# Optimization experiments

Hardware: AMD Instinct MI355X
Metric: run time of the kernel (lower is better)

Reference implementation:

```python
import jax, jax.numpy as jnp
import numpy as np

FACTOR = 2  # upsample factor per spatial dim


def setup_inputs() -> dict:
    key = jax.random.key(0)
    k1, k2, k3 = jax.random.split(key, 3)
    B, C_in, C_out, H, W_ = 8, 128, 128, 64, 64
    x = jax.random.normal(k1, (B, C_in, H, W_), dtype=jnp.float32)
    # conv3x3 params (OIHW), fan-in scaled init like torch Conv2d default scale
    fan_in = C_in * 3 * 3
    W = jax.random.normal(k2, (C_out, C_in, 3, 3), dtype=jnp.float32) / np.sqrt(fan_in)
    b = jax.random.normal(k3, (C_out,), dtype=jnp.float32) * 0.01
    return {"x": x, "W": W, "b": b}


def reference(x, W, b):
    h = jnp.repeat(jnp.repeat(x, FACTOR, axis=2), FACTOR, axis=3)  # [B,C,2H,2W]
    # conv3x3: stride 1, padding 1
    out = jax.lax.conv_general_dilated(
        h, W,
        window_strides=(1, 1),
        padding=((1, 1), (1, 1)),
        dimension_numbers=("NCHW", "OIHW", "NCHW"),
    )
    return out + b[None, :, None, None]
```

## Files before the change

kernel.cpp:

```cpp
#include <hip/hip_runtime.h>
#include <stdint.h>

typedef short bf16x8 __attribute__((ext_vector_type(8)));
typedef float f32x4 __attribute__((ext_vector_type(4)));
typedef float f32x16 __attribute__((ext_vector_type(16)));

#define NCI 128
#define NCO 128
#define HIN 64
#define NB  8

__device__ __forceinline__ unsigned short f32_to_bf16(float f) {
    union { float f; uint32_t u; } v; v.f = f;
    return (unsigned short)((v.u + 0x7FFFu + ((v.u >> 16) & 1u)) >> 16);
}

__device__ __forceinline__ void gl_lds16(const void* g, void* l) {
    __builtin_amdgcn_global_load_lds(
        (const __attribute__((address_space(1))) unsigned int*)g,
        (__attribute__((address_space(3))) unsigned int*)l, 16, 0, 0);
}

__device__ __forceinline__ float weff_sum(const float* wp, int py, int px, int ty, int tx) {
    float s = 0.f;
    #pragma unroll
    for (int ky = 0; ky < 3; ++ky) {
        bool iy = (py == 0) ? (ty == 0 ? (ky == 0) : (ky >= 1))
                            : (ty == 0 ? (ky <= 1) : (ky == 2));
        if (!iy) continue;
        #pragma unroll
        for (int kx = 0; kx < 3; ++kx) {
            bool ix = (px == 0) ? (tx == 0 ? (kx == 0) : (kx >= 1))
                                : (tx == 0 ? (kx <= 1) : (kx == 2));
            if (ix) s += wp[ky * 3 + kx];
        }
    }
    return s;
}

__global__ __launch_bounds__(256) void prep_kernel(
        const float* __restrict__ W, const float* __restrict__ x,
        unsigned short* __restrict__ Aw9, unsigned short* __restrict__ xq) {
    if (blockIdx.x < 1024) {
        int idx = blockIdx.x * 256 + threadIdx.x;
        int e   = idx & 7;
        int l   = (idx >> 3) & 63;
        int fm  = (idx >> 9) & 1;
        int s   = (idx >> 10) & 31;
        int coh = (idx >> 15) & 1;
        int par = idx >> 16;
        int co = coh * 64 + fm * 32 + (l & 31);
        int k  = s * 16 + (l >> 5) * 8 + e;
        int tap = k >> 7, ci = k & 127;
        Aw9[idx] = f32_to_bf16(weff_sum(W + (co * NCI + ci) * 9,
                                        par >> 1, par & 1, tap >> 1, tap & 1));
    } else {
        const int bb = blockIdx.x - 1024;
        const int b = bb / 66, hp = bb % 66;
        const int t = threadIdx.x;
        unsigned short* rowp = xq + ((((size_t)b * 4) * 66 + hp) * 64) * 32;
        if (hp == 0 || hp == 65) {
            bf16x8 z = (bf16x8){0, 0, 0, 0, 0, 0, 0, 0};
            for (int i = t; i < 1024; i += 256) {
                int g = i >> 8, rem = i & 255;
                int w = rem >> 2, q = rem & 3;
                *(bf16x8*)(xq + (((((size_t)(b * 4 + g)) * 66 + hp) * 64 + w) << 5) + q * 8) = z;
            }
            return;
        }
        const int h = hp - 1;
        const int w = t & 63, g = t >> 6;
        const float* src = x + ((size_t)(b * NCI + g * 32) * (HIN * HIN)) + h * HIN + w;
        unsigned short* dst = xq + (((((size_t)(b * 4 + g)) * 66 + hp) * 64 + w) << 5);
        #pragma unroll
        for (int q = 0; q < 4; ++q) {
            bf16x8 v;
            #pragma unroll
            for (int j = 0; j < 8; ++j)
                v[j] = (short)f32_to_bf16(src[(size_t)(q * 8 + j) * (HIN * HIN)]);
            *(bf16x8*)(dst + q * 8) = v;
        }
    }
}

__global__ __launch_bounds__(256, 2) void upconv17_kernel(
        const unsigned short* __restrict__ xq, const unsigned short* __restrict__ Aw9,
        const float* __restrict__ bv, float* __restrict__ out) {
    __shared__ __align__(16) unsigned short B_lds[40960];
    const int d = blockIdx.x;
    const int bi  = d & 7;
    const int py  = (d >> 3) & 1;
    const int px  = (d >> 4) & 1;
    const int coh = (d >> 5) & 1;
    const int ys  = d >> 6;
    const int tid = threadIdx.x, lane = tid & 63, ol = tid >> 6;
    const int l31 = lane & 31, lh = lane >> 5;
    const int par = py * 2 + px;

    #pragma unroll
    for (int i = 0; i < 20; ++i) {
        const int u = i * 256 + tid;
        const int qs = u & 15, cell = u >> 4;
        const int r = cell >> 6, w = cell & 63;
        const int q = qs ^ (w & 15);
        const int hp = ys * 4 + py + r;
        const unsigned short* gb = xq +
            (((((size_t)(bi * 4 + (q >> 2))) * 66 + hp) * 64 + w) << 5) + (q & 3) * 8;
        gl_lds16(gb, &B_lds[u * 8]);
    }

    const unsigned short* Ag = Aw9 + (((size_t)(par * 2 + coh)) << 15);
    bf16x8 Abuf[3][2];
    auto loadA = [&](bf16x8* Ad, int s) {
        const unsigned short* p = Ag + (s << 10) + lane * 8;
        Ad[0] = *(const bf16x8*)p;
        Ad[1] = *(const bf16x8*)(p + 512);
    };
    loadA(Abuf[0], 0);
    loadA(Abuf[1], 1);
    loadA(Abuf[2], 2);
    asm volatile("s_waitcnt vmcnt(0)" ::: "memory");
    __builtin_amdgcn_s_barrier();

    f32x16 acc[2][2];
    #pragma unroll
    for (int i = 0; i < 2; ++i)
        #pragma unroll
        for (int j = 0; j < 2; ++j)
            #pragma unroll
            for (int q = 0; q < 16; ++q)
                acc[i][j][q] = 0.f;

    #pragma unroll
    for (int s = 0; s < 32; ++s) {
        bf16x8* Ac = Abuf[s % 3];
        const int ty = s >> 4, tx = (s >> 3) & 1;
        const int q = (s & 7) * 2 + lh;
        const int r = ol + ty;
        __builtin_amdgcn_s_setprio(1);
        #pragma unroll
        for (int fn = 0; fn < 2; ++fn) {
            const int wr = fn * 32 + l31 + px + tx - 1;
            const bool valid = (unsigned)wr < 64u;
            const int w = valid ? wr : 0;
            const int qs = q ^ (w & 15);
            bf16x8 bfr = *(const bf16x8*)&B_lds[(((r << 6) + w) * 16 + qs) * 8];
            bfr = valid ? bfr : (bf16x8){0, 0, 0, 0, 0, 0, 0, 0};
            #pragma unroll
            for (int fm = 0; fm < 2; ++fm)
                acc[fm][fn] = __builtin_amdgcn_mfma_f32_32x32x16_bf16(
                    Ac[fm], bfr, acc[fm][fn], 0, 0, 0);
        }
        __builtin_amdgcn_s_setprio(0);
        if (s + 3 < 32) loadA(Abuf[s % 3], s + 3);
    }

    const int yy = 2 * (ys * 4 + ol) + py;
    #pragma unroll
    for (int fm = 0; fm < 2; ++fm) {
        #pragma unroll
        for (int fn = 0; fn < 2; ++fn) {
            const int xx = 2 * (fn * 32 + l31) + px;
            #pragma unroll
            for (int j = 0; j < 16; ++j) {
                const int row = (j & 3) + 8 * (j >> 2) + 4 * lh;
                const int co = coh * 64 + fm * 32 + row;
                out[(((size_t)(bi * NCO + co)) << 14) + yy * 128 + xx] =
                    acc[fm][fn][j] + bv[co];
            }
        }
    }
}

__global__ void weff_flat_kernel(const float* __restrict__ W,
                                 unsigned short* __restrict__ Aw) {
    int idx = blockIdx.x * 256 + threadIdx.x;
    int par = idx >> 16;
    int co  = (idx >> 9) & 127;
    int k   = idx & 511;
    int tap = k >> 7, ci = k & 127;
    Aw[idx] = f32_to_bf16(weff_sum(W + (co * NCI + ci) * 9,
                                   par >> 1, par & 1, tap >> 1, tap & 1));
}

__global__ __launch_bounds__(256) void upconv_fb_kernel(
        const float* __restrict__ x, const unsigned short* __restrict__ Aw,
        const float* __restrict__ bv, float* __restrict__ out) {
    __shared__ __align__(16) unsigned short A_lds[128 * 32];
    __shared__ __align__(16) unsigned short B_lds[128 * 32];
    const int par = blockIdx.y, py = par >> 1, px = par & 1;
    const int s0 = blockIdx.x * 128;
    const int bimg = s0 >> 12;
    const int oy0 = (s0 >> 6) & 63;
    const int tid = threadIdx.x;
    const int lane = tid & 63, wave = tid >> 6;
    const int wm = wave >> 1, wn = wave & 1;
    const float* xb = x + bimg * (NCI * HIN * HIN);
    f32x4 acc[4][4];
    #pragma unroll
    for (int i = 0; i < 4; ++i)
        #pragma unroll
        for (int j = 0; j < 4; ++j)
            acc[i][j] = (f32x4){0.f, 0.f, 0.f, 0.f};
    for (int kt = 0; kt < 16; ++kt) {
        const int tap = kt >> 2, ci0 = (kt & 3) * 32;
        const int ty = tap >> 1, tx = tap & 1;
        #pragma unroll
        for (int i = 0; i < 2; ++i) {
            int c = i * 256 + tid;
            *(bf16x8*)(&A_lds[c * 8]) = *(const bf16x8*)(Aw +
                ((par * 128 + (c >> 2)) * 512 + kt * 32 + (c & 3) * 8));
        }
        #pragma unroll
        for (int i = 0; i < 2; ++i) {
            int tsk = i * 256 + tid;
            int n = tsk & 127, kg = tsk >> 7;
            int r = n >> 6, ox = n & 63;
            int row = oy0 + r - 1 + py + ty;
            int col = ox - 1 + px + tx;
            bool ok = (row >= 0) & (row < HIN) & (col >= 0) & (col < HIN);
            const float* xp = xb + (((ci0 + kg * 8) * HIN + row) * HIN + col);
            bf16x8 v;
            #pragma unroll
            for (int q = 0; q < 8; ++q) {
                float f = ok ? xp[q * (HIN * HIN)] : 0.f;
                v[q] = (short)f32_to_bf16(f);
            }
            *(bf16x8*)(&B_lds[n * 32 + kg * 8]) = v;
        }
        __syncthreads();
        const int seg = (lane >> 4) * 8, rl2 = lane & 15;
        bf16x8 af[4], bfr[4];
        #pragma unroll
        for (int f = 0; f < 4; ++f)
            af[f] = *(const bf16x8*)(&A_lds[(wm * 64 + f * 16 + rl2) * 32 + seg]);
        #pragma unroll
        for (int f = 0; f < 4; ++f)
            bfr[f] = *(const bf16x8*)(&B_lds[(wn * 64 + f * 16 + rl2) * 32 + seg]);
        #pragma unroll
        for (int fm = 0; fm < 4; ++fm)
            #pragma unroll
            for (int fn = 0; fn < 4; ++fn)
                acc[fm][fn] = __builtin_amdgcn_mfma_f32_16x16x32_bf16(
                    af[fm], bfr[fn], acc[fm][fn], 0, 0, 0);
        __syncthreads();
    }
    #pragma unroll
    for (int fm = 0; fm < 4; ++fm) {
        const int co_b = wm * 64 + fm * 16 + (lane >> 4) * 4;
        float bias4[4];
        #pragma unroll
        for (int j = 0; j < 4; ++j) bias4[j] = bv[co_b + j];
        #pragma unroll
        for (int fn = 0; fn < 4; ++fn) {
            int n = wn * 64 + fn * 16 + (lane & 15);
            int s = s0 + n;
            int ox = s & 63, oy = (s >> 6) & 63, bi2 = s >> 12;
            int yy = 2 * oy + py, xx = 2 * ox + px;
            float* op = out + ((size_t)bi2 * 128 * 128 * 128) + (size_t)yy * 128 + xx;
            #pragma unroll
            for (int j = 0; j < 4; ++j)
                op[(size_t)(co_b + j) * (128 * 128)] = acc[fm][fn][j] + bias4[j];
        }
    }
}

extern "C" void kernel_launch(void* const* d_in, const int* in_sizes, int n_in,
                              void* d_out, int out_size, void* d_ws, size_t ws_size,
                              hipStream_t stream) {
    const float* x  = (const float*)d_in[0];
    const float* W  = (const float*)d_in[1];
    const float* bv = (const float*)d_in[2];
    float* out = (float*)d_out;
    unsigned short* Aw = (unsigned short*)d_ws;
    const size_t aw_bytes = (size_t)4 * 2 * 32 * 2 * 512 * sizeof(unsigned short);
    const size_t xq_bytes = (size_t)NB * 4 * 66 * 64 * 32 * sizeof(unsigned short);

    if (ws_size >= aw_bytes + xq_bytes) {
        unsigned short* xq = (unsigned short*)((char*)d_ws + aw_bytes);
        prep_kernel<<<1024 + 528, 256, 0, stream>>>(W, x, Aw, xq);
        upconv17_kernel<<<1024, 256, 0, stream>>>(xq, Aw, bv, out);
    } else {
        weff_flat_kernel<<<1024, 256, 0, stream>>>(W, Aw);
        upconv_fb_kernel<<<dim3(256, 4), 256, 0, stream>>>(x, Aw, bv, out);
    }
}
```

Before: 41.24 us.

## Make upconv blocks process four tiles sequentially with 256-block grid

Each block now loops over two output-channel halves and two row strips, reusing the staged LDS input tile across both channel halves instead of launching one block per tile. The grid shrinks from 1024 to 256 blocks (about one per CU) and the launch bound is relaxed to one block per SM. This cuts redundant B staging and block launch overhead, but removes inter-block latency hiding and serializes the second B staging behind barriers.

```diff
diff --git a/kernel.cpp b/kernel.cpp
--- a/kernel.cpp
+++ b/kernel.cpp
@@ -58,7 +58,6 @@
         const int bb = blockIdx.x - 1024;
         const int b = bb / 66, hp = bb % 66;
         const int t = threadIdx.x;
-        unsigned short* rowp = xq + ((((size_t)b * 4) * 66 + hp) * 64) * 32;
         if (hp == 0 || hp == 65) {
             bf16x8 z = (bf16x8){0, 0, 0, 0, 0, 0, 0, 0};
             for (int i = t; i < 1024; i += 256) {
@@ -83,7 +82,7 @@
     }
 }
 
-__global__ __launch_bounds__(256, 2) void upconv17_kernel(
+__global__ __launch_bounds__(256, 1) void upconv18_kernel(
         const unsigned short* __restrict__ xq, const unsigned short* __restrict__ Aw9,
         const float* __restrict__ bv, float* __restrict__ out) {
     __shared__ __align__(16) unsigned short B_lds[40960];
@@ -91,82 +90,98 @@
     const int bi  = d & 7;
     const int py  = (d >> 3) & 1;
     const int px  = (d >> 4) & 1;
-    const int coh = (d >> 5) & 1;
-    const int ys  = d >> 6;
+    const int ysp = d >> 5;
     const int tid = threadIdx.x, lane = tid & 63, ol = tid >> 6;
     const int l31 = lane & 31, lh = lane >> 5;
     const int par = py * 2 + px;
 
-    #pragma unroll
-    for (int i = 0; i < 20; ++i) {
-        const int u = i * 256 + tid;
-        const int qs = u & 15, cell = u >> 4;
-        const int r = cell >> 6, w = cell & 63;
-        const int q = qs ^ (w & 15);
-        const int hp = ys * 4 + py + r;
-        const unsigned short* gb = xq +
-            (((((size_t)(bi * 4 + (q >> 2))) * 66 + hp) * 64 + w) << 5) + (q & 3) * 8;
-        gl_lds16(gb, &B_lds[u * 8]);
-    }
-
-    const unsigned short* Ag = Aw9 + (((size_t)(par * 2 + coh)) << 15);
-    bf16x8 Abuf[3][2];
-    auto loadA = [&](bf16x8* Ad, int s) {
-        const unsigned short* p = Ag + (s << 10) + lane * 8;
-        Ad[0] = *(const bf16x8*)p;
-        Ad[1] = *(const bf16x8*)(p + 512);
+    auto stageB = [&](int st) {
+        #pragma unroll
+        for (int i = 0; i < 20; ++i) {
+            const int u = i * 256 + tid;
+            const int qs = u & 15, cell = u >> 4;
+            const int r = cell >> 6, w = cell & 63;
+            const int q = qs ^ (w & 15);
+            const int hp = st * 4 + py + r;
+            const unsigned short* gb = xq +
+                (((((size_t)(bi * 4 + (q >> 2))) * 66 + hp) * 64 + w) << 5) + (q & 3) * 8;
+            gl_lds16(gb, &B_lds[u * 8]);
+        }
     };
-    loadA(Abuf[0], 0);
-    loadA(Abuf[1], 1);
-    loadA(Abuf[2], 2);
+
+    stageB(2 * ysp);
     asm volatile("s_waitcnt vmcnt(0)" ::: "memory");
     __builtin_amdgcn_s_barrier();
 
-    f32x16 acc[2][2];
-    #pragma unroll
-    for (int i = 0; i < 2; ++i)
-        #pragma unroll
-        for (int j = 0; j < 2; ++j)
-            #pragma unroll
-            for (int q = 0; q < 16; ++q)
-                acc[i][j][q] = 0.f;
-
-    #pragma unroll
-    for (int s = 0; s < 32; ++s) {
-        bf16x8* Ac = Abuf[s % 3];
-        const int ty = s >> 4, tx = (s >> 3) & 1;
-        const int q = (s & 7) * 2 + lh;
-        const int r = ol + ty;
-        __builtin_amdgcn_s_setprio(1);
-        #pragma unroll
-        for (int fn = 0; fn < 2; ++fn) {
-            const int wr = fn * 32 + l31 + px + tx - 1;
-            const bool valid = (unsigned)wr < 64u;
-            const int w = valid ? wr : 0;
-            const int qs = q ^ (w & 15);
-            bf16x8 bfr = *(const bf16x8*)&B_lds[(((r << 6) + w) * 16 + qs) * 8];
-            bfr = valid ? bfr : (bf16x8){0, 0, 0, 0, 0, 0, 0, 0};
-            #pragma unroll
-            for (int fm = 0; fm < 2; ++fm)
-                acc[fm][fn] = __builtin_amdgcn_mfma_f32_32x32x16_bf16(
-                    Ac[fm], bfr, acc[fm][fn], 0, 0, 0);
-        }
-        __builtin_amdgcn_s_setprio(0);
-        if (s + 3 < 32) loadA(Abuf[s % 3], s + 3);
-    }
-
-    const int yy = 2 * (ys * 4 + ol) + py;
-    #pragma unroll
-    for (int fm = 0; fm < 2; ++fm) {
-        #pragma unroll
-        for (int fn = 0; fn < 2; ++fn) {
-            const int xx = 2 * (fn * 32 + l31) + px;
-            #pragma unroll
-            for (int j = 0; j < 16; ++j) {
-                const int row = (j & 3) + 8 * (j >> 2) + 4 * lh;
-                const int co = coh * 64 + fm * 32 + row;
-                out[(((size_t)(bi * NCO + co)) << 14) + yy * 128 + xx] =
-                    acc[fm][fn][j] + bv[co];
+    for (int t = 0; t < 4; ++t) {
+        const int coh = t & 1;
+        const int st = 2 * ysp + (t >> 1);
+        if (t == 2) {
+            __builtin_amdgcn_s_barrier();
+            stageB(st);
+            asm volatile("s_waitcnt vmcnt(0)" ::: "memory");
+            __builtin_amdgcn_s_barrier();
+        }
+
+        const unsigned short* Ag = Aw9 + (((size_t)(par * 2 + coh)) << 15);
+        bf16x8 Abuf[3][2];
+        #pragma unroll
+        for (int i = 0; i < 3; ++i) {
+            const unsigned short* p = Ag + (i << 10) + lane * 8;
+            Abuf[i][0] = *(const bf16x8*)p;
+            Abuf[i][1] = *(const bf16x8*)(p + 512);
+        }
+
+        f32x16 acc[2][2];
+        #pragma unroll
+        for (int i = 0; i < 2; ++i)
+            #pragma unroll
+            for (int j = 0; j < 2; ++j)
+                #pragma unroll
+                for (int q = 0; q < 16; ++q)
+                    acc[i][j][q] = 0.f;
+
+        #pragma unroll
+        for (int s = 0; s < 32; ++s) {
+            bf16x8* Ac = Abuf[s % 3];
+            const int ty = s >> 4, tx = (s >> 3) & 1;
+            const int q = (s & 7) * 2 + lh;
+            const int r = ol + ty;
+            __builtin_amdgcn_s_setprio(1);
+            #pragma unroll
+            for (int fn = 0; fn < 2; ++fn) {
+                const int wr = fn * 32 + l31 + px + tx - 1;
+                const bool valid = (unsigned)wr < 64u;
+                const int w = valid ? wr : 0;
+                const int qs = q ^ (w & 15);
+                bf16x8 bfr = *(const bf16x8*)&B_lds[(((r << 6) + w) * 16 + qs) * 8];
+                bfr = valid ? bfr : (bf16x8){0, 0, 0, 0, 0, 0, 0, 0};
+                #pragma unroll
+                for (int fm = 0; fm < 2; ++fm)
+                    acc[fm][fn] = __builtin_amdgcn_mfma_f32_32x32x16_bf16(
+                        Ac[fm], bfr, acc[fm][fn], 0, 0, 0);
+            }
+            __builtin_amdgcn_s_setprio(0);
+            if (s + 3 < 32) {
+                const unsigned short* p = Ag + ((s + 3) << 10) + lane * 8;
+                Abuf[s % 3][0] = *(const bf16x8*)p;
+                Abuf[s % 3][1] = *(const bf16x8*)(p + 512);
+            }
+        }
+
+        const int yy = 2 * (st * 4 + ol) + py;
+        #pragma unroll
+        for (int fm = 0; fm < 2; ++fm) {
+            #pragma unroll
+            for (int fn = 0; fn < 2; ++fn) {
+                const int xx = 2 * (fn * 32 + l31) + px;
+                #pragma unroll
+                for (int j = 0; j < 16; ++j) {
+                    const int row = (j & 3) + 8 * (j >> 2) + 4 * lh;
+                    const int co = (t & 1) * 64 + fm * 32 + row;
+                    out[(((size_t)(bi * NCO + co)) << 14) + yy * 128 + xx] =
+                        acc[fm][fn][j] + bv[co];
+                }
             }
         }
     }
@@ -279,7 +294,7 @@
     if (ws_size >= aw_bytes + xq_bytes) {
         unsigned short* xq = (unsigned short*)((char*)d_ws + aw_bytes);
         prep_kernel<<<1024 + 528, 256, 0, stream>>>(W, x, Aw, xq);
-        upconv17_kernel<<<1024, 256, 0, stream>>>(xq, Aw, bv, out);
+        upconv18_kernel<<<256, 256, 0, stream>>>(xq, Aw, bv, out);
     } else {
         weff_flat_kernel<<<1024, 256, 0, stream>>>(W, Aw);
         upconv_fb_kernel<<<dim3(256, 4), 256, 0, stream>>>(x, Aw, bv, out);
```

Measured after the change: 46.21 us. 12.1% more time.

## Fuse input bf16 conversion into conv kernel, drop xq staging buffer

Applied to the files above, without the earlier changes.

Removes the separate pre-pass that converted x into a padded, channel-grouped bf16 buffer. The main kernel now reads fp32 x directly, converts it to bf16 and writes it into swizzled LDS, with zero padding handled by predication. This drops one round trip through global memory and shrinks the prep kernel to weight folding only. In exchange each block does strided scalar fp32 loads and conversions itself, rather than async direct-to-LDS copies, and input rows are re-read by several blocks.

```diff
diff --git a/kernel.cpp b/kernel.cpp
--- a/kernel.cpp
+++ b/kernel.cpp
@@ -15,12 +15,6 @@
     return (unsigned short)((v.u + 0x7FFFu + ((v.u >> 16) & 1u)) >> 16);
 }
 
-__device__ __forceinline__ void gl_lds16(const void* g, void* l) {
-    __builtin_amdgcn_global_load_lds(
-        (const __attribute__((address_space(1))) unsigned int*)g,
-        (__attribute__((address_space(3))) unsigned int*)l, 16, 0, 0);
-}
-
 __device__ __forceinline__ float weff_sum(const float* wp, int py, int px, int ty, int tx) {
     float s = 0.f;
     #pragma unroll
@@ -38,53 +32,24 @@
     return s;
 }
 
-__global__ __launch_bounds__(256) void prep_kernel(
-        const float* __restrict__ W, const float* __restrict__ x,
-        unsigned short* __restrict__ Aw9, unsigned short* __restrict__ xq) {
-    if (blockIdx.x < 1024) {
-        int idx = blockIdx.x * 256 + threadIdx.x;
-        int e   = idx & 7;
-        int l   = (idx >> 3) & 63;
-        int fm  = (idx >> 9) & 1;
-        int s   = (idx >> 10) & 31;
-        int coh = (idx >> 15) & 1;
-        int par = idx >> 16;
-        int co = coh * 64 + fm * 32 + (l & 31);
-        int k  = s * 16 + (l >> 5) * 8 + e;
-        int tap = k >> 7, ci = k & 127;
-        Aw9[idx] = f32_to_bf16(weff_sum(W + (co * NCI + ci) * 9,
-                                        par >> 1, par & 1, tap >> 1, tap & 1));
-    } else {
-        const int bb = blockIdx.x - 1024;
-        const int b = bb / 66, hp = bb % 66;
-        const int t = threadIdx.x;
-        unsigned short* rowp = xq + ((((size_t)b * 4) * 66 + hp) * 64) * 32;
-        if (hp == 0 || hp == 65) {
-            bf16x8 z = (bf16x8){0, 0, 0, 0, 0, 0, 0, 0};
-            for (int i = t; i < 1024; i += 256) {
-                int g = i >> 8, rem = i & 255;
-                int w = rem >> 2, q = rem & 3;
-                *(bf16x8*)(xq + (((((size_t)(b * 4 + g)) * 66 + hp) * 64 + w) << 5) + q * 8) = z;
-            }
-            return;
-        }
-        const int h = hp - 1;
-        const int w = t & 63, g = t >> 6;
-        const float* src = x + ((size_t)(b * NCI + g * 32) * (HIN * HIN)) + h * HIN + w;
-        unsigned short* dst = xq + (((((size_t)(b * 4 + g)) * 66 + hp) * 64 + w) << 5);
-        #pragma unroll
-        for (int q = 0; q < 4; ++q) {
-            bf16x8 v;
-            #pragma unroll
-            for (int j = 0; j < 8; ++j)
-                v[j] = (short)f32_to_bf16(src[(size_t)(q * 8 + j) * (HIN * HIN)]);
-            *(bf16x8*)(dst + q * 8) = v;
-        }
-    }
-}
-
-__global__ __launch_bounds__(256, 2) void upconv17_kernel(
-        const unsigned short* __restrict__ xq, const unsigned short* __restrict__ Aw9,
+__global__ __launch_bounds__(256) void weff9_kernel(
+        const float* __restrict__ W, unsigned short* __restrict__ Aw9) {
+    int idx = blockIdx.x * 256 + threadIdx.x;
+    int e   = idx & 7;
+    int l   = (idx >> 3) & 63;
+    int fm  = (idx >> 9) & 1;
+    int s   = (idx >> 10) & 31;
+    int coh = (idx >> 15) & 1;
+    int par = idx >> 16;
+    int co = coh * 64 + fm * 32 + (l & 31);
+    int k  = s * 16 + (l >> 5) * 8 + e;
+    int tap = k >> 7, ci = k & 127;
+    Aw9[idx] = f32_to_bf16(weff_sum(W + (co * NCI + ci) * 9,
+                                    par >> 1, par & 1, tap >> 1, tap & 1));
+}
+
+__global__ __launch_bounds__(256, 2) void upconv19_kernel(
+        const float* __restrict__ x, const unsigned short* __restrict__ Aw9,
         const float* __restrict__ bv, float* __restrict__ out) {
     __shared__ __align__(16) unsigned short B_lds[40960];
     const int d = blockIdx.x;
@@ -93,34 +58,36 @@
     const int px  = (d >> 4) & 1;
     const int coh = (d >> 5) & 1;
     const int ys  = d >> 6;
-    const int tid = threadIdx.x, lane = tid & 63, ol = tid >> 6;
+    const int tid = threadIdx.x, lane = tid & 63, wv = tid >> 6, ol = wv;
     const int l31 = lane & 31, lh = lane >> 5;
     const int par = py * 2 + px;
 
-    #pragma unroll
-    for (int i = 0; i < 20; ++i) {
-        const int u = i * 256 + tid;
-        const int qs = u & 15, cell = u >> 4;
-        const int r = cell >> 6, w = cell & 63;
-        const int q = qs ^ (w & 15);
-        const int hp = ys * 4 + py + r;
-        const unsigned short* gb = xq +
-            (((((size_t)(bi * 4 + (q >> 2))) * 66 + hp) * 64 + w) << 5) + (q & 3) * 8;
-        gl_lds16(gb, &B_lds[u * 8]);
-    }
-
     const unsigned short* Ag = Aw9 + (((size_t)(par * 2 + coh)) << 15);
     bf16x8 Abuf[3][2];
-    auto loadA = [&](bf16x8* Ad, int s) {
-        const unsigned short* p = Ag + (s << 10) + lane * 8;
-        Ad[0] = *(const bf16x8*)p;
-        Ad[1] = *(const bf16x8*)(p + 512);
-    };
-    loadA(Abuf[0], 0);
-    loadA(Abuf[1], 1);
-    loadA(Abuf[2], 2);
-    asm volatile("s_waitcnt vmcnt(0)" ::: "memory");
-    __builtin_amdgcn_s_barrier();
+    #pragma unroll
+    for (int i = 0; i < 3; ++i) {
+        const unsigned short* p = Ag + (i << 10) + lane * 8;
+        Abuf[i][0] = *(const bf16x8*)p;
+        Abuf[i][1] = *(const bf16x8*)(p + 512);
+    }
+
+    #pragma unroll
+    for (int i = 0; i < 20; ++i) {
+        const int tk = i * 4 + wv;
+        const int r = tk >> 4, o = tk & 15;
+        const int grow = ys * 4 + py + r - 1;
+        const bool ok = (unsigned)grow < 64u;
+        const float* xp = x + ((size_t)(bi * NCI + o * 8) * HIN + (ok ? grow : 0)) * HIN + lane;
+        bf16x8 v;
+        #pragma unroll
+        for (int j = 0; j < 8; ++j) {
+            float f = ok ? xp[(size_t)j * (HIN * HIN)] : 0.f;
+            v[j] = (short)f32_to_bf16(f);
+        }
+        const int w = lane;
+        *(bf16x8*)&B_lds[(((r << 6) + w) * 16 + (o ^ (w & 15))) * 8] = v;
+    }
+    __syncthreads();
 
     f32x16 acc[2][2];
     #pragma unroll
@@ -152,7 +119,11 @@
                     Ac[fm], bfr, acc[fm][fn], 0, 0, 0);
         }
         __builtin_amdgcn_s_setprio(0);
-        if (s + 3 < 32) loadA(Abuf[s % 3], s + 3);
+        if (s + 3 < 32) {
+            const unsigned short* p = Ag + ((s + 3) << 10) + lane * 8;
+            Abuf[s % 3][0] = *(const bf16x8*)p;
+            Abuf[s % 3][1] = *(const bf16x8*)(p + 512);
+        }
     }
 
     const int yy = 2 * (ys * 4 + ol) + py;
@@ -274,12 +245,10 @@
     float* out = (float*)d_out;
     unsigned short* Aw = (unsigned short*)d_ws;
     const size_t aw_bytes = (size_t)4 * 2 * 32 * 2 * 512 * sizeof(unsigned short);
-    const size_t xq_bytes = (size_t)NB * 4 * 66 * 64 * 32 * sizeof(unsigned short);
-
-    if (ws_size >= aw_bytes + xq_bytes) {
-        unsigned short* xq = (unsigned short*)((char*)d_ws + aw_bytes);
-        prep_kernel<<<1024 + 528, 256, 0, stream>>>(W, x, Aw, xq);
-        upconv17_kernel<<<1024, 256, 0, stream>>>(xq, Aw, bv, out);
+
+    if (ws_size >= aw_bytes) {
+        weff9_kernel<<<1024, 256, 0, stream>>>(W, Aw);
+        upconv19_kernel<<<1024, 256, 0, stream>>>(x, Aw, bv, out);
     } else {
         weff_flat_kernel<<<1024, 256, 0, stream>>>(W, Aw);
         upconv_fb_kernel<<<dim3(256, 4), 256, 0, stream>>>(x, Aw, bv, out);
```

After: 53.07 us. 1.29x slower.
